# Performance work log

Measured on AMD Instinct MI355X. Metric: run time of the kernel, lower is better.

Reference implementation:

```python
import jax, jax.numpy as jnp
import numpy as np

B, N, S, D1, D2 = 16, 4096, 1024, 64, 256
IN_CH, OUT_CH = D1 + D2, 256
BN_EPS = 1e-5


def setup_inputs() -> dict:
    key = jax.random.key(0)
    ks = jax.random.split(key, 5)
    xyz1 = jax.random.normal(ks[0], (B, N, 3), dtype=jnp.float32)
    xyz2 = jax.random.normal(ks[1], (B, S, 3), dtype=jnp.float32)
    points1 = jax.random.normal(ks[2], (B, D1, N), dtype=jnp.float32)
    points2 = jax.random.normal(ks[3], (B, D2, S), dtype=jnp.float32)
    # Conv1d(kernel_size=1, bias=False) weight, squeezed to [out, in]
    W = jax.random.normal(ks[4], (OUT_CH, IN_CH), dtype=jnp.float32) * 0.05
    gamma = jnp.ones((OUT_CH,), dtype=jnp.float32)
    beta = jnp.zeros((OUT_CH,), dtype=jnp.float32)
    return dict(xyz1=xyz1, xyz2=xyz2, points1=points1, points2=points2,
                W=W, gamma=gamma, beta=beta)


def reference(xyz1, xyz2, points1, points2, W, gamma, beta):
    # --- three_nn: squared pairwise distances [B, N, S] + top-3 nearest ---
    d2 = (jnp.sum(xyz1 * xyz1, axis=-1, keepdims=True)          # [B,N,1]
          + jnp.sum(xyz2 * xyz2, axis=-1)[:, None, :]            # [B,1,S]
          - 2.0 * jnp.einsum('bnd,bsd->bns', xyz1, xyz2))        # [B,N,S]
    neg_d, idx = jax.lax.top_k(-d2, 3)                           # [B,N,3]
    dists = -neg_d
    # inverse-distance weights
    dist_recip = 1.0 / (dists + 1e-8)
    weight = dist_recip / jnp.sum(dist_recip, axis=2, keepdims=True)  # [B,N,3]
    # --- three_interpolate: gather + weighted sum ---
    p2 = jnp.swapaxes(points2, 1, 2)                             # [B,S,C]
    gathered = jax.vmap(lambda p, i: p[i])(p2, idx)              # [B,N,3,C]
    interp = jnp.einsum('bnkc,bnk->bcn', gathered, weight)       # [B,C,N]
    # --- concat skip features + ConvBNReLU1D (1x1 conv, bias=False) ---
    x = jnp.concatenate([points1, interp], axis=1)               # [B,IN_CH,N]
    y = jnp.einsum('oc,bcn->bon', W, x)                          # [B,OUT_CH,N]
    # BatchNorm1d in training mode: biased batch stats over (B, N)
    mean = jnp.mean(y, axis=(0, 2), keepdims=True)
    var = jnp.mean(jnp.square(y - mean), axis=(0, 2), keepdims=True)
    y = (y - mean) * jax.lax.rsqrt(var + BN_EPS)
    y = y * gamma[None, :, None] + beta[None, :, None]
    return jax.nn.relu(y)
```

## Files before the change

### kernel.cpp

```cpp
#include <hip/hip_runtime.h>
#include <stdint.h>


#define B_   16
#define N_   4096
#define S_   1024
#define D1_  64
#define D2_  256
#define OC_  256

typedef __attribute__((ext_vector_type(8))) short bf16x8;
typedef __attribute__((ext_vector_type(4))) float f32x4;
typedef __attribute__((ext_vector_type(4))) unsigned int u32x4;
typedef __attribute__((ext_vector_type(2))) unsigned int u32x2;

#define IDXW_OFF 0u
#define ZTB_OFF  2097152u
#define Y1_OFF   10485760u
#define Y2_OFF   44040192u
#define PART_OFF 77594624u
#define W1B_OFF  77662208u
#define W2B_OFF  77694976u
#define WS_NEED  77826048u

__device__ __forceinline__ uint16_t f2bf(float f) {
    union { float f; uint32_t u; } v; v.f = f;
    uint32_t r = v.u + 0x7FFFu + ((v.u >> 16) & 1u);
    return (uint16_t)(r >> 16);
}
__device__ __forceinline__ float bf2f(uint32_t h) {
    union { uint32_t u; float f; } v; v.u = h << 16;
    return v.f;
}

#define INSERT(d, sidx, d0, d1, d2, i0, i1, i2) do {                      \
    bool ca = (d) < (d2); bool cb = (d) < (d1); bool cc = (d) < (d0);     \
    float _n1 = __builtin_amdgcn_fmed3f((d), (d0), (d1));                 \
    float _n2 = __builtin_amdgcn_fmed3f((d), (d1), (d2));                 \
    int _j2 = cb ? (i1) : (ca ? (sidx) : (i2));                           \
    int _j1 = cc ? (i0) : (cb ? (sidx) : (i1));                           \
    i0 = cc ? (sidx) : (i0);                                              \
    d0 = fminf((d), (d0)); d1 = _n1; d2 = _n2; i1 = _j1; i2 = _j2;        \
} while (0)

__global__ void __launch_bounds__(256, 8)
k01(const float* __restrict__ xyz1, const float* __restrict__ xyz2,
    int* __restrict__ idxw, const float* __restrict__ W,
    uint16_t* __restrict__ w1b, uint16_t* __restrict__ w2b) {
    __shared__ float4 pts[8 * 129];
    int i = blockIdx.x;
    int t = threadIdx.x;
    if (i >= 2048) {
        int e = (i - 2048) * 256 + t;
        if (e < OC_ * 320) {
            int o = e / 320, c = e % 320;
            uint16_t b = f2bf(W[e]);
            if (c < 64) w1b[o * 64 + c] = b;
            else        w2b[o * 256 + (c - 64)] = b;
        }
        return;
    }
    int b  = i >> 7;
    int n0 = (i & 127) * 32;

    for (int s = t; s < S_; s += 256) {
        const float* p = xyz2 + ((size_t)b * S_ + s) * 3;
        pts[(s >> 7) * 129 + (s & 127)] = make_float4(p[0], p[1], p[2], 0.f);
    }
    __syncthreads();

    int chunk = t & 7, nidx = t >> 3;
    int n = n0 + nidx;
    const float* q = xyz1 + ((size_t)b * N_ + n) * 3;
    float ax = q[0], ay = q[1], az = q[2];

    float d0 = 3.4e38f, d1 = 3.4e38f, d2 = 3.4e38f;
    int   i0 = 0, i1 = 0, i2 = 0;

    const float4* base = pts + chunk * 129;
    int sbase = chunk * 128;
    #pragma unroll 4
    for (int j = 0; j < 128; j++) {
        float4 qq = base[j];
        int s = sbase + j;
        float dx = ax - qq.x, dy = ay - qq.y, dz = az - qq.z;
        float d = fmaf(dz, dz, fmaf(dy, dy, dx * dx));
        INSERT(d, s, d0, d1, d2, i0, i1, i2);
    }
    #pragma unroll
    for (int m = 1; m <= 4; m <<= 1) {
        float e0 = __shfl_xor(d0, m), e1 = __shfl_xor(d1, m), e2 = __shfl_xor(d2, m);
        int   g0 = __shfl_xor(i0, m), g1 = __shfl_xor(i1, m), g2 = __shfl_xor(i2, m);
        INSERT(e0, g0, d0, d1, d2, i0, i1, i2);
        INSERT(e1, g1, d0, d1, d2, i0, i1, i2);
        INSERT(e2, g2, d0, d1, d2, i0, i1, i2);
    }
    if (chunk == 0) {
        float r0 = 1.0f / (d0 + 1e-8f), r1 = 1.0f / (d1 + 1e-8f), r2 = 1.0f / (d2 + 1e-8f);
        float rs = r0 + r1 + r2;
        float* fw = (float*)idxw;
        int bb = (b * N_ + n) * 8;
        idxw[bb + 0] = i0; idxw[bb + 1] = i1; idxw[bb + 2] = i2;
        fw[bb + 4] = r0 / rs; fw[bb + 5] = r1 / rs; fw[bb + 6] = r2 / rs;
    }
}

__global__ void __launch_bounds__(256, 4)
k2f(const float* __restrict__ p2, const uint16_t* __restrict__ w2b,
    uint16_t* __restrict__ ztb, const float* __restrict__ p1,
    const uint16_t* __restrict__ w1b, uint16_t* __restrict__ y1) {
    __shared__ char smem[40960];
    int i = blockIdx.x;
    int t = threadIdx.x, l = t & 63, w = t >> 6;
    if (i < 256) {
        uint16_t* a_t = (uint16_t*)smem;
        uint16_t* w_t = (uint16_t*)(smem + 8192);
        int b = i >> 4, s0 = (i & 15) * 64;

        f32x4 acc[4][4] = {};
        for (int ck = 0; ck < 4; ck++) {
            __syncthreads();
            {
                int sA = w * 16 + (l & 15);
                const float* p2b = p2 + ((size_t)b * D2_ + (size_t)ck * 64) * S_ + s0;
                #pragma unroll
                for (int j = 0; j < 8; j++) {
                    int cp = (l >> 4) + 4 * j;
                    float lo = p2b[(size_t)(2 * cp) * S_ + sA];
                    float hi = p2b[(size_t)(2 * cp + 1) * S_ + sA];
                    uint32_t pk = (uint32_t)f2bf(lo) | ((uint32_t)f2bf(hi) << 16);
                    *(uint32_t*)((char*)a_t + sA * 128 + ((cp * 4) ^ ((sA & 7) << 4))) = pk;
                }
            }
            {
                int wp = t & 31, orow0 = t >> 5;
                #pragma unroll 4
                for (int jj = 0; jj < 32; jj++) {
                    int o = orow0 + 8 * jj;
                    uint32_t v = *(const uint32_t*)(w2b + (size_t)o * 256 + ck * 64 + 2 * wp);
                    *(uint32_t*)((char*)w_t + o * 128 + ((wp * 4) ^ ((o & 7) << 4))) = v;
                }
            }
            __syncthreads();
            #pragma unroll
            for (int ks = 0; ks < 2; ks++) {
                bf16x8 a[4], bb[4];
                int co = ks * 32 + (l >> 4) * 8;
                #pragma unroll
                for (int mi = 0; mi < 4; mi++) {
                    int s = mi * 16 + (l & 15);
                    a[mi] = *(const bf16x8*)((const char*)a_t + s * 128 + ((co * 2) ^ ((s & 7) << 4)));
                }
                #pragma unroll
                for (int oj = 0; oj < 4; oj++) {
                    int o = w * 64 + oj * 16 + (l & 15);
                    bb[oj] = *(const bf16x8*)((const char*)w_t + o * 128 + ((co * 2) ^ ((o & 7) << 4)));
                }
                #pragma unroll
                for (int mi = 0; mi < 4; mi++)
                    #pragma unroll
                    for (int oj = 0; oj < 4; oj++)
                        acc[mi][oj] = __builtin_amdgcn_mfma_f32_16x16x32_bf16(
                            a[mi], bb[oj], acc[mi][oj], 0, 0, 0);
            }
        }
        __syncthreads();
        char* tz = smem;
        #pragma unroll
        for (int mi = 0; mi < 4; mi++)
            #pragma unroll
            for (int oj = 0; oj < 4; oj++)
                #pragma unroll
                for (int r = 0; r < 4; r++) {
                    int sl = mi * 16 + (l >> 4) * 4 + r;
                    int o  = w * 64 + oj * 16 + (l & 15);
                    *(uint16_t*)(tz + sl * 512 + ((o * 2) ^ ((sl & 7) << 5))) = f2bf(acc[mi][oj][r]);
                }
        __syncthreads();
        {
            int og = t >> 4, rr = t & 15;
            uint16_t* zb = ztb + ((size_t)(b * 16 + og) * S_ + s0) * 16;
            #pragma unroll
            for (int k = 0; k < 4; k++) {
                int s = rr * 4 + k;
                u32x4 v0 = *(u32x4*)(tz + s * 512 + ((og * 32) ^ ((s & 7) << 5)));
                u32x4 v1 = *(u32x4*)(tz + s * 512 + (((og * 32) ^ ((s & 7) << 5)) | 16));
                __builtin_nontemporal_store(v0, (u32x4*)(zb + (size_t)s * 16));
                __builtin_nontemporal_store(v1, (u32x4*)(zb + (size_t)s * 16 + 8));
            }
        }
    } else {
        int j2 = i - 256;
        int b = j2 >> 7, n0 = (j2 & 127) * 32;
        int oW = w * 64;
        uint16_t* pt = (uint16_t*)smem;
        {
            int nn = t & 31;
            const float* p1b = p1 + (size_t)b * D1_ * N_ + n0;
            #pragma unroll
            for (int j = 0; j < 4; j++) {
                int cp = (t >> 5) + 8 * j;
                float lo = p1b[(size_t)(2 * cp) * N_ + nn];
                float hi = p1b[(size_t)(2 * cp + 1) * N_ + nn];
                uint32_t pk = (uint32_t)f2bf(lo) | ((uint32_t)f2bf(hi) << 16);
                *(uint32_t*)((char*)pt + nn * 128 + ((cp * 4) ^ ((nn & 7) << 4))) = pk;
            }
        }
        bf16x8 af[2][4];
        #pragma unroll
        for (int ks = 0; ks < 2; ks++)
            #pragma unroll
            for (int mi = 0; mi < 4; mi++) {
                int o = oW + mi * 16 + (l & 15);
                af[ks][mi] = *(const bf16x8*)(w1b + (size_t)o * 64 + ks * 32 + (l >> 4) * 8);
            }
        f32x4 acc[4][2] = {};
        __syncthreads();
        #pragma unroll
        for (int ks = 0; ks < 2; ks++) {
            bf16x8 bf[2];
            int co = ks * 32 + (l >> 4) * 8;
            #pragma unroll
            for (int bj = 0; bj < 2; bj++) {
                int nn = bj * 16 + (l & 15);
                bf[bj] = *(const bf16x8*)((const char*)pt + nn * 128 + ((co * 2) ^ ((nn & 7) << 4)));
            }
            #pragma unroll
            for (int mi = 0; mi < 4; mi++)
                #pragma unroll
                for (int bj = 0; bj < 2; bj++)
                    acc[mi][bj] = __builtin_amdgcn_mfma_f32_16x16x32_bf16(
                        af[ks][mi], bf[bj], acc[mi][bj], 0, 0, 0);
        }
        #pragma unroll
        for (int mi = 0; mi < 4; mi++) {
            int og = w * 4 + mi;
            uint16_t* yb = y1 + ((size_t)(b * 16 + og)) * N_ * 16;
            #pragma unroll
            for (int bj = 0; bj < 2; bj++) {
                int n = n0 + bj * 16 + (l & 15);
                int oo = (l >> 4) * 4;
                u32x2 v;
                v.x = (uint32_t)f2bf(acc[mi][bj][0]) | ((uint32_t)f2bf(acc[mi][bj][1]) << 16);
                v.y = (uint32_t)f2bf(acc[mi][bj][2]) | ((uint32_t)f2bf(acc[mi][bj][3]) << 16);
                __builtin_nontemporal_store(v, (u32x2*)(yb + (size_t)n * 16 + oo));
            }
        }
    }
}

__global__ void __launch_bounds__(1024, 8)
k3a(const uint16_t* __restrict__ y1, const uint16_t* __restrict__ ztb,
    const int* __restrict__ idxw, uint16_t* __restrict__ y2,
    float* __restrict__ partials) {
    __shared__ char zsm[49152];
    __shared__ float red[16][16][2];
    int bi = blockIdx.x;
    int b = bi >> 5, og = (bi >> 1) & 15, nh = bi & 1;
    int u = threadIdx.x, l = u & 63, w = u >> 6;
    {
        const u32x4* src = (const u32x4*)(ztb + ((size_t)(b * 16 + og)) * S_ * 16);
        #pragma unroll
        for (int k = 0; k < 2; k++) {
            int g = k * 1024 + u;
            u32x4 v = src[g];
            *(u32x4*)(zsm + (g >> 1) * 48 + (g & 1) * 16) = v;
        }
    }
    __syncthreads();
    int q = l >> 2, sub = l & 3;
    float s1l[4] = {0.f, 0.f, 0.f, 0.f}, s2l[4] = {0.f, 0.f, 0.f, 0.f};
    int nbase = nh * 2048 + w * 128;
    const uint16_t* y1b = y1 + ((size_t)(b * 16 + og)) * N_ * 16;
    uint16_t* y2b = y2 + ((size_t)(b * 16 + og)) * N_ * 16;
    #pragma unroll 2
    for (int it = 0; it < 8; it++) {
        int n = nbase + it * 16 + q;
        u32x2 y1v = __builtin_nontemporal_load((const u32x2*)(y1b + (size_t)n * 16 + sub * 4));
        const int* ib = idxw + ((size_t)(b * N_ + n)) * 8;
        int4   iv = *(const int4*)ib;
        float4 wv = *((const float4*)ib + 1);
        u32x2 z0 = *(const u32x2*)(zsm + iv.x * 48 + sub * 8);
        u32x2 z1 = *(const u32x2*)(zsm + iv.y * 48 + sub * 8);
        u32x2 z2 = *(const u32x2*)(zsm + iv.z * 48 + sub * 8);
        float a0 = bf2f(y1v.x & 0xffff) + wv.x * bf2f(z0.x & 0xffff) + wv.y * bf2f(z1.x & 0xffff) + wv.z * bf2f(z2.x & 0xffff);
        float a1 = bf2f(y1v.x >> 16)    + wv.x * bf2f(z0.x >> 16)    + wv.y * bf2f(z1.x >> 16)    + wv.z * bf2f(z2.x >> 16);
        float a2 = bf2f(y1v.y & 0xffff) + wv.x * bf2f(z0.y & 0xffff) + wv.y * bf2f(z1.y & 0xffff) + wv.z * bf2f(z2.y & 0xffff);
        float a3 = bf2f(y1v.y >> 16)    + wv.x * bf2f(z0.y >> 16)    + wv.y * bf2f(z1.y >> 16)    + wv.z * bf2f(z2.y >> 16);
        s1l[0] += a0; s2l[0] += a0 * a0;
        s1l[1] += a1; s2l[1] += a1 * a1;
        s1l[2] += a2; s2l[2] += a2 * a2;
        s1l[3] += a3; s2l[3] += a3 * a3;
        u32x2 vv;
        vv.x = (uint32_t)f2bf(a0) | ((uint32_t)f2bf(a1) << 16);
        vv.y = (uint32_t)f2bf(a2) | ((uint32_t)f2bf(a3) << 16);
        __builtin_nontemporal_store(vv, (u32x2*)(y2b + (size_t)n * 16 + sub * 4));
    }
    #pragma unroll
    for (int m = 4; m <= 32; m <<= 1)
        #pragma unroll
        for (int j = 0; j < 4; j++) {
            s1l[j] += __shfl_xor(s1l[j], m);
            s2l[j] += __shfl_xor(s2l[j], m);
        }
    if (l < 4) {
        #pragma unroll
        for (int j = 0; j < 4; j++) {
            red[w][sub * 4 + j][0] = s1l[j];
            red[w][sub * 4 + j][1] = s2l[j];
        }
    }
    __syncthreads();
    if (u < 32) {
        int oi = u >> 1, st = u & 1;
        float s = 0.f;
        #pragma unroll
        for (int ww = 0; ww < 16; ww++) s += red[ww][oi][st];
        partials[(size_t)bi * 32 + oi * 2 + st] = s;
    }
}

__global__ void __launch_bounds__(256, 8)
k3c(const uint16_t* __restrict__ y2, const float* __restrict__ partials,
    const float* __restrict__ gamma, const float* __restrict__ beta,
    float* __restrict__ out) {
    __shared__ uint16_t ty[16 * 256];
    __shared__ float stat[32];
    __shared__ float sbsh[32];
    int bi = blockIdx.x;
    int b = bi >> 8, og = (bi >> 4) & 15, nc = bi & 15;
    int u = threadIdx.x;
    const uint16_t* src = y2 + (((size_t)(b * 16 + og)) * N_ + nc * 256) * 16;
    u32x4 va = __builtin_nontemporal_load((const u32x4*)(src + (size_t)u * 16));
    u32x4 vb = __builtin_nontemporal_load((const u32x4*)(src + (size_t)u * 16 + 8));
    if (u < 32) {
        int oi = u >> 1, st = u & 1;
        float s = 0.f;
        #pragma unroll 4
        for (int t2 = 0; t2 < 32; t2++) {
            int row = (t2 >> 1) * 32 + og * 2 + (t2 & 1);
            s += partials[(size_t)row * 32 + oi * 2 + st];
        }
        stat[u] = s;
    }
    __syncthreads();
    if (u < 16) {
        float mean = stat[u * 2] / 65536.0f;
        float var  = stat[u * 2 + 1] / 65536.0f - mean * mean;
        int o_g = og * 16 + u;
        float scale = gamma[o_g] * rsqrtf(var + 1e-5f);
        sbsh[u * 2]     = scale;
        sbsh[u * 2 + 1] = beta[o_g] - mean * scale;
    }
    uint32_t words[8] = {va.x, va.y, va.z, va.w, vb.x, vb.y, vb.z, vb.w};
    #pragma unroll
    for (int h = 0; h < 8; h++) {
        int o0 = h * 2, o1 = h * 2 + 1;
        *(uint16_t*)((char*)ty + o0 * 512 + ((u * 2) ^ ((o0 & 7) << 4))) = (uint16_t)(words[h] & 0xffff);
        *(uint16_t*)((char*)ty + o1 * 512 + ((u * 2) ^ ((o1 & 7) << 4))) = (uint16_t)(words[h] >> 16);
    }
    __syncthreads();
    int o = u >> 4, k = u & 15;
    int x = (o & 7) << 4;
    int o_g = og * 16 + o;
    float scale = sbsh[o * 2], bias = sbsh[o * 2 + 1];
    float* dst = out + ((size_t)(b * OC_ + o_g)) * N_ + nc * 256;
    #pragma unroll
    for (int g2 = 0; g2 < 4; g2++) {
        uint64_t z = *(const uint64_t*)((const char*)ty + o * 512 + ((g2 * 128 + k * 8) ^ x));
        f32x4 r;
        r.x = fmaxf(0.f, fmaf(bf2f((uint32_t)(z       ) & 0xffff), scale, bias));
        r.y = fmaxf(0.f, fmaf(bf2f((uint32_t)(z >> 16 ) & 0xffff), scale, bias));
        r.z = fmaxf(0.f, fmaf(bf2f((uint32_t)(z >> 32 ) & 0xffff), scale, bias));
        r.w = fmaxf(0.f, fmaf(bf2f((uint32_t)(z >> 48 ) & 0xffff), scale, bias));
        __builtin_nontemporal_store(r, (f32x4*)(dst + g2 * 64 + k * 4));
    }
}

extern "C" void kernel_launch(void* const* d_in, const int* in_sizes, int n_in,
                              void* d_out, int out_size, void* d_ws, size_t ws_size,
                              hipStream_t stream) {
    const float* xyz1  = (const float*)d_in[0];
    const float* xyz2  = (const float*)d_in[1];
    const float* p1    = (const float*)d_in[2];
    const float* p2    = (const float*)d_in[3];
    const float* W     = (const float*)d_in[4];
    const float* gamma = (const float*)d_in[5];
    const float* beta  = (const float*)d_in[6];
    float* out = (float*)d_out;
    char* ws = (char*)d_ws;
    if (ws_size < (size_t)WS_NEED) return;

    int*      idxw     = (int*)(ws + IDXW_OFF);
    uint16_t* ztb      = (uint16_t*)(ws + ZTB_OFF);
    uint16_t* y1       = (uint16_t*)(ws + Y1_OFF);
    uint16_t* y2       = (uint16_t*)(ws + Y2_OFF);
    float*    partials = (float*)(ws + PART_OFF);
    uint16_t* w1b      = (uint16_t*)(ws + W1B_OFF);
    uint16_t* w2b      = (uint16_t*)(ws + W2B_OFF);

    hipLaunchKernelGGL(k01, dim3(2368), dim3(256),  0, stream,
                       xyz1, xyz2, idxw, W, w1b, w2b);
    hipLaunchKernelGGL(k2f, dim3(2304), dim3(256),  0, stream,
                       p2, w2b, ztb, p1, w1b, y1);
    hipLaunchKernelGGL(k3a, dim3(512),  dim3(1024), 0, stream,
                       y1, ztb, idxw, y2, partials);
    hipLaunchKernelGGL(k3c, dim3(4096), dim3(256),  0, stream,
                       y2, partials, gamma, beta, out);
}
```

Baseline: 109.7 us.

## Restructure points2 projection GEMM into smaller tiles with direct weight loads

The points2×W2 projection branch of k2f now uses 32-column tiles (512 blocks instead of 256) and stages the full 256-channel activation slice in LDS once, removing the 4-step K loop and its barriers. Weight fragments are read straight from global memory instead of being staged in LDS, and results are written directly as bf16 scalars rather than through an LDS transpose with nontemporal vector stores. Shared memory drops to 16 KB and launch bounds rise to 8 blocks per CU to raise occupancy. The trade-off is uncoalesced 2-byte global stores and repeated global weight reads that depend on cache hits.

```diff
diff --git a/kernel.cpp b/kernel.cpp
--- a/kernel.cpp
+++ b/kernel.cpp
@@ -105,92 +105,58 @@
     }
 }
 
-__global__ void __launch_bounds__(256, 4)
+__global__ void __launch_bounds__(256, 8)
 k2f(const float* __restrict__ p2, const uint16_t* __restrict__ w2b,
     uint16_t* __restrict__ ztb, const float* __restrict__ p1,
     const uint16_t* __restrict__ w1b, uint16_t* __restrict__ y1) {
-    __shared__ char smem[40960];
+    __shared__ char smem[16384];
     int i = blockIdx.x;
     int t = threadIdx.x, l = t & 63, w = t >> 6;
-    if (i < 256) {
+    if (i < 512) {
         uint16_t* a_t = (uint16_t*)smem;
-        uint16_t* w_t = (uint16_t*)(smem + 8192);
-        int b = i >> 4, s0 = (i & 15) * 64;
-
-        f32x4 acc[4][4] = {};
-        for (int ck = 0; ck < 4; ck++) {
-            __syncthreads();
-            {
-                int sA = w * 16 + (l & 15);
-                const float* p2b = p2 + ((size_t)b * D2_ + (size_t)ck * 64) * S_ + s0;
+        int b = i >> 5, s0 = (i & 31) * 32;
+        int sA = t & 31, cpg = t >> 5;
+        const float* p2b = p2 + (size_t)b * D2_ * S_ + s0;
+        #pragma unroll
+        for (int j = 0; j < 16; j++) {
+            int cp = cpg + 8 * j;
+            float lo = p2b[(size_t)(2 * cp) * S_ + sA];
+            float hi = p2b[(size_t)(2 * cp + 1) * S_ + sA];
+            uint32_t pk = (uint32_t)f2bf(lo) | ((uint32_t)f2bf(hi) << 16);
+            *(uint32_t*)((char*)a_t + sA * 512 + ((cp * 4) ^ ((sA & 7) << 4))) = pk;
+        }
+        __syncthreads();
+        f32x4 acc[2][4] = {};
+        int ls = l & 15, swzs = (ls & 7) << 4;
+        #pragma unroll
+        for (int ks = 0; ks < 8; ks++) {
+            int co = ks * 32 + (l >> 4) * 8;
+            bf16x8 a0 = *(const bf16x8*)((const char*)a_t + ls * 512 + ((co * 2) ^ swzs));
+            bf16x8 a1 = *(const bf16x8*)((const char*)a_t + (16 + ls) * 512 + ((co * 2) ^ swzs));
+            bf16x8 bbf[4];
+            #pragma unroll
+            for (int oj = 0; oj < 4; oj++) {
+                int o = w * 64 + oj * 16 + ls;
+                bbf[oj] = *(const bf16x8*)(w2b + (size_t)o * 256 + co);
+            }
+            #pragma unroll
+            for (int oj = 0; oj < 4; oj++) {
+                acc[0][oj] = __builtin_amdgcn_mfma_f32_16x16x32_bf16(a0, bbf[oj], acc[0][oj], 0, 0, 0);
+                acc[1][oj] = __builtin_amdgcn_mfma_f32_16x16x32_bf16(a1, bbf[oj], acc[1][oj], 0, 0, 0);
+            }
+        }
+        #pragma unroll
+        for (int mi = 0; mi < 2; mi++)
+            #pragma unroll
+            for (int oj = 0; oj < 4; oj++) {
+                int og = w * 4 + oj;
+                uint16_t* zb = ztb + ((size_t)(b * 16 + og) * S_ + s0 + mi * 16 + (l >> 4) * 4) * 16 + ls;
                 #pragma unroll
-                for (int j = 0; j < 8; j++) {
-                    int cp = (l >> 4) + 4 * j;
-                    float lo = p2b[(size_t)(2 * cp) * S_ + sA];
-                    float hi = p2b[(size_t)(2 * cp + 1) * S_ + sA];
-                    uint32_t pk = (uint32_t)f2bf(lo) | ((uint32_t)f2bf(hi) << 16);
-                    *(uint32_t*)((char*)a_t + sA * 128 + ((cp * 4) ^ ((sA & 7) << 4))) = pk;
-                }
-            }
-            {
-                int wp = t & 31, orow0 = t >> 5;
-                #pragma unroll 4
-                for (int jj = 0; jj < 32; jj++) {
-                    int o = orow0 + 8 * jj;
-                    uint32_t v = *(const uint32_t*)(w2b + (size_t)o * 256 + ck * 64 + 2 * wp);
-                    *(uint32_t*)((char*)w_t + o * 128 + ((wp * 4) ^ ((o & 7) << 4))) = v;
-                }
-            }
-            __syncthreads();
-            #pragma unroll
-            for (int ks = 0; ks < 2; ks++) {
-                bf16x8 a[4], bb[4];
-                int co = ks * 32 + (l >> 4) * 8;
-                #pragma unroll
-                for (int mi = 0; mi < 4; mi++) {
-                    int s = mi * 16 + (l & 15);
-                    a[mi] = *(const bf16x8*)((const char*)a_t + s * 128 + ((co * 2) ^ ((s & 7) << 4)));
-                }
-                #pragma unroll
-                for (int oj = 0; oj < 4; oj++) {
-                    int o = w * 64 + oj * 16 + (l & 15);
-                    bb[oj] = *(const bf16x8*)((const char*)w_t + o * 128 + ((co * 2) ^ ((o & 7) << 4)));
-                }
-                #pragma unroll
-                for (int mi = 0; mi < 4; mi++)
-                    #pragma unroll
-                    for (int oj = 0; oj < 4; oj++)
-                        acc[mi][oj] = __builtin_amdgcn_mfma_f32_16x16x32_bf16(
-                            a[mi], bb[oj], acc[mi][oj], 0, 0, 0);
-            }
-        }
-        __syncthreads();
-        char* tz = smem;
-        #pragma unroll
-        for (int mi = 0; mi < 4; mi++)
-            #pragma unroll
-            for (int oj = 0; oj < 4; oj++)
-                #pragma unroll
-                for (int r = 0; r < 4; r++) {
-                    int sl = mi * 16 + (l >> 4) * 4 + r;
-                    int o  = w * 64 + oj * 16 + (l & 15);
-                    *(uint16_t*)(tz + sl * 512 + ((o * 2) ^ ((sl & 7) << 5))) = f2bf(acc[mi][oj][r]);
-                }
-        __syncthreads();
-        {
-            int og = t >> 4, rr = t & 15;
-            uint16_t* zb = ztb + ((size_t)(b * 16 + og) * S_ + s0) * 16;
-            #pragma unroll
-            for (int k = 0; k < 4; k++) {
-                int s = rr * 4 + k;
-                u32x4 v0 = *(u32x4*)(tz + s * 512 + ((og * 32) ^ ((s & 7) << 5)));
-                u32x4 v1 = *(u32x4*)(tz + s * 512 + (((og * 32) ^ ((s & 7) << 5)) | 16));
-                __builtin_nontemporal_store(v0, (u32x4*)(zb + (size_t)s * 16));
-                __builtin_nontemporal_store(v1, (u32x4*)(zb + (size_t)s * 16 + 8));
-            }
-        }
+                for (int r = 0; r < 4; r++)
+                    zb[(size_t)r * 16] = f2bf(acc[mi][oj][r]);
+            }
     } else {
-        int j2 = i - 256;
+        int j2 = i - 512;
         int b = j2 >> 7, n0 = (j2 & 127) * 32;
         int oW = w * 64;
         uint16_t* pt = (uint16_t*)smem;
@@ -401,7 +367,7 @@
 
     hipLaunchKernelGGL(k01, dim3(2368), dim3(256),  0, stream,
                        xyz1, xyz2, idxw, W, w1b, w2b);
-    hipLaunchKernelGGL(k2f, dim3(2304), dim3(256),  0, stream,
+    hipLaunchKernelGGL(k2f, dim3(2560), dim3(256),  0, stream,
                        p2, w2b, ztb, p1, w1b, y1);
     hipLaunchKernelGGL(k3a, dim3(512),  dim3(1024), 0, stream,
                        y1, ztb, idxw, y2, partials);
```

New measurement: 100.5 us. 8.4% less time.
